# Kernel tuning notes

Measured on AMD Instinct MI355X. Metric: run time of the kernel, lower is better.

## Reference

```python
import jax, jax.numpy as jnp
import numpy as np

N_NODES = 100000
N_EDGES = 1600000
N_CONCEPTS = 500000
D = 128  # concept_dim = graph_hidden_dim = graph_output_dim


def setup_inputs() -> dict:
    key = jax.random.key(0)
    ks = jax.random.split(key, 10)
    cncpt_ids = jax.random.randint(ks[0], (N_NODES,), 0, N_CONCEPTS)
    src = jax.random.randint(ks[1], (N_EDGES,), 0, N_NODES)
    dst = jax.random.randint(ks[2], (N_EDGES,), 0, N_NODES)
    emb_table = jax.random.normal(ks[3], (N_CONCEPTS, D), dtype=jnp.float32)
    W1 = jax.random.normal(ks[4], (D, D), dtype=jnp.float32) * 0.05
    b1 = jax.random.normal(ks[5], (D,), dtype=jnp.float32) * 0.05
    W2 = jax.random.normal(ks[6], (D, D), dtype=jnp.float32) * 0.05
    b2 = jax.random.normal(ks[7], (D,), dtype=jnp.float32) * 0.05
    Wout = jax.random.normal(ks[8], (1, D), dtype=jnp.float32) * 0.05
    bout = jax.random.normal(ks[9], (1,), dtype=jnp.float32) * 0.05
    return {"cncpt_ids": cncpt_ids, "src": src, "dst": dst,
            "emb_table": emb_table, "W1": W1, "b1": b1,
            "W2": W2, "b2": b2, "Wout": Wout, "bout": bout}


def _gcn_layer(h, src, dst, W, b, n_nodes):
    # DGL update_all(copy_src, sum): gather messages from src, sum into dst
    agg = jax.ops.segment_sum(h[src], dst, num_segments=n_nodes)  # [N, d_in]
    return jax.nn.relu(agg @ W.T + b)  # NodeApplyModule: Linear + ReLU


def reference(cncpt_ids, src, dst, emb_table, W1, b1, W2, b2, Wout, bout):
    n_nodes = cncpt_ids.shape[0]
    h = emb_table[cncpt_ids]                       # [N, D] concept embeddings
    h = _gcn_layer(h, src, dst, W1, b1, n_nodes)   # gcn1
    h = _gcn_layer(h, src, dst, W2, b2, n_nodes)   # gcn2
    x = h[None]                                    # torch.stack([h]) -> [1, N, D]
    logits = jax.nn.sigmoid(x @ Wout.T + bout)     # hidden2output -> [1, N, 1]
    return logits
```

## Files before the change

### kernel.cpp

```cpp
#include <hip/hip_runtime.h>
#include <math.h>

#define D 128
#define SCAN_B 256

typedef __attribute__((ext_vector_type(8))) short bfrag;
typedef __attribute__((ext_vector_type(4))) float ffrag;

__device__ inline unsigned short f2bf(float f) {
    unsigned u = __float_as_uint(f);
    u += 0x7FFF + ((u >> 16) & 1);
    return (unsigned short)(u >> 16);
}
__device__ inline float bf2f(unsigned short h) {
    return __uint_as_float(((unsigned)h) << 16);
}
__device__ inline unsigned pack_bf2(float a, float b) {
    return ((unsigned)f2bf(a)) | (((unsigned)f2bf(b)) << 16);
}

__global__ void setup1_kernel(const float* __restrict__ W1,
                              const float* __restrict__ W2,
                              unsigned short* __restrict__ hi1,
                              unsigned short* __restrict__ lo1,
                              unsigned short* __restrict__ hi2,
                              unsigned short* __restrict__ lo2,
                              int* __restrict__ deg, int np1, int nblk_w) {
    if ((int)blockIdx.x < nblk_w) {
        int i = blockIdx.x * blockDim.x + threadIdx.x;
        if (i < D * D) {
            float f1 = W1[i];
            unsigned short h1 = f2bf(f1);
            hi1[i] = h1;
            lo1[i] = f2bf(f1 - bf2f(h1));
            float f2 = W2[i];
            unsigned short h2 = f2bf(f2);
            hi2[i] = h2;
            lo2[i] = f2bf(f2 - bf2f(h2));
        }
    } else {
        int i = ((int)blockIdx.x - nblk_w) * blockDim.x + threadIdx.x;
        if (i < np1) deg[i] = 0;
    }
}

__global__ void setup2_kernel(const float* __restrict__ emb,
                              const int* __restrict__ ids,
                              uint4* __restrict__ h4,
                              const int* __restrict__ dst,
                              int* __restrict__ deg,
                              int n_nodes, int n_edges, int nblk_g) {
    if ((int)blockIdx.x < nblk_g) {
        int idx = blockIdx.x * blockDim.x + threadIdx.x;
        int total = n_nodes * 16;
        if (idx >= total) return;
        int node = idx >> 4;
        int c = idx & 15;
        size_t cid = (size_t)ids[node];
        const float4* s = (const float4*)(emb + cid * D) + c * 2;
        float4 v0 = s[0];
        float4 v1 = s[1];
        uint4 p;
        p.x = pack_bf2(v0.x, v0.y);
        p.y = pack_bf2(v0.z, v0.w);
        p.z = pack_bf2(v1.x, v1.y);
        p.w = pack_bf2(v1.z, v1.w);
        h4[(size_t)node * 16 + c] = p;
    } else {
        int e = ((int)blockIdx.x - nblk_g) * blockDim.x + threadIdx.x;
        if (e < n_edges) atomicAdd(&deg[dst[e]], 1);
    }
}

__global__ __launch_bounds__(SCAN_B) void scan_block_kernel(
        const int* __restrict__ deg, int* __restrict__ row_ptr,
        int* __restrict__ blocksums, int n) {
    __shared__ int s[SCAN_B];
    int i = blockIdx.x * SCAN_B + threadIdx.x;
    int v = (i < n) ? deg[i] : 0;
    s[threadIdx.x] = v;
    __syncthreads();
    #pragma unroll
    for (int off = 1; off < SCAN_B; off <<= 1) {
        int t = (threadIdx.x >= off) ? s[threadIdx.x - off] : 0;
        __syncthreads();
        s[threadIdx.x] += t;
        __syncthreads();
    }
    if (i < n) row_ptr[i] = s[threadIdx.x] - v;
    if (threadIdx.x == SCAN_B - 1) blocksums[blockIdx.x] = s[SCAN_B - 1];
}

__global__ __launch_bounds__(512) void scan_sums_kernel(int* __restrict__ blocksums,
                                                        int nb) {
    __shared__ int s[512];
    int v = (threadIdx.x < nb) ? blocksums[threadIdx.x] : 0;
    s[threadIdx.x] = v;
    __syncthreads();
    #pragma unroll
    for (int off = 1; off < 512; off <<= 1) {
        int t = (threadIdx.x >= off) ? s[threadIdx.x - off] : 0;
        __syncthreads();
        s[threadIdx.x] += t;
        __syncthreads();
    }
    if (threadIdx.x < nb) blocksums[threadIdx.x] = s[threadIdx.x] - v;
}

__global__ void add_offsets_kernel(int* __restrict__ row_ptr,
                                   const int* __restrict__ blocksums,
                                   int* __restrict__ cursor, int n, int n_nodes) {
    int i = blockIdx.x * blockDim.x + threadIdx.x;
    if (i >= n) return;
    int rp = row_ptr[i] + blocksums[i / SCAN_B];
    row_ptr[i] = rp;
    if (i < n_nodes) cursor[i] = rp;
}

__global__ void csr_fill_kernel(const int* __restrict__ src,
                                const int* __restrict__ dst,
                                int* __restrict__ cursor,
                                int* __restrict__ esrc, int n_edges) {
    int e = blockIdx.x * blockDim.x + threadIdx.x;
    if (e >= n_edges) return;
    int pos = atomicAdd(&cursor[dst[e]], 1);
    esrc[pos] = src[e];
}

#define ACC8(u) do { \
    a0 += __uint_as_float((u).x << 16); a1 += __uint_as_float((u).x & 0xffff0000u); \
    a2 += __uint_as_float((u).y << 16); a3 += __uint_as_float((u).y & 0xffff0000u); \
    a4 += __uint_as_float((u).z << 16); a5 += __uint_as_float((u).z & 0xffff0000u); \
    a6 += __uint_as_float((u).w << 16); a7 += __uint_as_float((u).w & 0xffff0000u); \
} while (0)

__global__ __launch_bounds__(256) void agg_kernel(
        const uint4* __restrict__ h4, const int* __restrict__ row_ptr,
        const int* __restrict__ esrc, uint4* __restrict__ agg4, int n_nodes) {
    int node = blockIdx.x * 4 + (threadIdx.x >> 6);
    int lane = threadIdx.x & 63;
    if (node >= n_nodes) return;
    const int c = lane & 15;
    const int g = lane >> 4;
    int beg = row_ptr[node], end = row_ptr[node + 1];
    int deg = end - beg;

    int myidx = 0;
    if (lane < deg) myidx = esrc[beg + lane];

    float a0 = 0.f, a1 = 0.f, a2 = 0.f, a3 = 0.f;
    float a4 = 0.f, a5 = 0.f, a6 = 0.f, a7 = 0.f;

    int nfast = deg < 64 ? deg : 64;
    for (int base = 0; base < nfast; base += 16) {
        int p0 = base + g;
        int s0 = __shfl(myidx, p0, 64);
        int s1 = __shfl(myidx, p0 + 4, 64);
        int s2 = __shfl(myidx, p0 + 8, 64);
        int s3 = __shfl(myidx, p0 + 12, 64);
        bool v0 = p0 < nfast;
        bool v1 = (p0 + 4) < nfast;
        bool v2 = (p0 + 8) < nfast;
        bool v3 = (p0 + 12) < nfast;
        uint4 u0, u1, u2, u3;
        if (v0) u0 = h4[(size_t)s0 * 16 + c];
        if (v1) u1 = h4[(size_t)s1 * 16 + c];
        if (v2) u2 = h4[(size_t)s2 * 16 + c];
        if (v3) u3 = h4[(size_t)s3 * 16 + c];
        if (v0) ACC8(u0);
        if (v1) ACC8(u1);
        if (v2) ACC8(u2);
        if (v3) ACC8(u3);
    }
    for (int i = beg + 64 + g; i < end; i += 4) {
        uint4 u = h4[(size_t)esrc[i] * 16 + c];
        ACC8(u);
    }

    a0 += __shfl_xor(a0, 16, 64); a0 += __shfl_xor(a0, 32, 64);
    a1 += __shfl_xor(a1, 16, 64); a1 += __shfl_xor(a1, 32, 64);
    a2 += __shfl_xor(a2, 16, 64); a2 += __shfl_xor(a2, 32, 64);
    a3 += __shfl_xor(a3, 16, 64); a3 += __shfl_xor(a3, 32, 64);
    a4 += __shfl_xor(a4, 16, 64); a4 += __shfl_xor(a4, 32, 64);
    a5 += __shfl_xor(a5, 16, 64); a5 += __shfl_xor(a5, 32, 64);
    a6 += __shfl_xor(a6, 16, 64); a6 += __shfl_xor(a6, 32, 64);
    a7 += __shfl_xor(a7, 16, 64); a7 += __shfl_xor(a7, 32, 64);

    if (g == 0) {
        uint4 r;
        r.x = pack_bf2(a0, a1);
        r.y = pack_bf2(a2, a3);
        r.z = pack_bf2(a4, a5);
        r.w = pack_bf2(a6, a7);
        agg4[(size_t)node * 16 + c] = r;
    }
}

__global__ __launch_bounds__(256) void linear_mfma_kernel(
        const unsigned short* __restrict__ x,
        const unsigned short* __restrict__ Whi,
        const unsigned short* __restrict__ Wlo,
        const float* __restrict__ b,
        unsigned short* __restrict__ y,
        const float* __restrict__ wout,
        const float* __restrict__ bout,
        float* __restrict__ outp,
        int n_nodes, int fuse_out) {
    __shared__ __align__(16) unsigned short sW[2][D][136];

    {
        const uint4* Wh4 = (const uint4*)Whi;
        const uint4* Wl4 = (const uint4*)Wlo;
        #pragma unroll
        for (int j = 0; j < 8; ++j) {
            int ch = (int)threadIdx.x + j * 256;
            int row = ch >> 4, k8 = ch & 15;
            *(uint4*)&sW[0][row][k8 * 8] = Wh4[ch];
            *(uint4*)&sW[1][row][k8 * 8] = Wl4[ch];
        }
    }
    __syncthreads();

    const int lane = threadIdx.x & 63;
    const int col  = lane & 15;
    const int quad = lane >> 4;
    const int wave = blockIdx.x * 4 + (threadIdx.x >> 6);
    const int nwaves = gridDim.x * 4;
    const int ngroups = (n_nodes + 15) >> 4;

    float bvals[8], wvals[8];
    #pragma unroll
    for (int nt = 0; nt < 8; ++nt) {
        bvals[nt] = b[nt * 16 + col];
        wvals[nt] = fuse_out ? wout[nt * 16 + col] : 0.f;
    }
    const float bout0 = fuse_out ? bout[0] : 0.f;

    for (int g = wave; g < ngroups; g += nwaves) {
        int node = g * 16 + col;
        int nload = node < n_nodes ? node : (n_nodes - 1);

        bfrag a[4];
        #pragma unroll
        for (int kt = 0; kt < 4; ++kt)
            a[kt] = *(const bfrag*)(x + (size_t)nload * D + kt * 32 + quad * 8);

        float part0 = 0.f, part1 = 0.f, part2 = 0.f, part3 = 0.f;

        #pragma unroll
        for (int nt = 0; nt < 8; ++nt) {
            ffrag c = {0.f, 0.f, 0.f, 0.f};
            #pragma unroll
            for (int kt = 0; kt < 4; ++kt) {
                bfrag bh = *(const bfrag*)&sW[0][nt * 16 + col][kt * 32 + quad * 8];
                bfrag bl = *(const bfrag*)&sW[1][nt * 16 + col][kt * 32 + quad * 8];
                c = __builtin_amdgcn_mfma_f32_16x16x32_bf16(a[kt], bh, c, 0, 0, 0);
                c = __builtin_amdgcn_mfma_f32_16x16x32_bf16(a[kt], bl, c, 0, 0, 0);
            }
            if (fuse_out) {
                part0 += fmaxf(c[0] + bvals[nt], 0.f) * wvals[nt];
                part1 += fmaxf(c[1] + bvals[nt], 0.f) * wvals[nt];
                part2 += fmaxf(c[2] + bvals[nt], 0.f) * wvals[nt];
                part3 += fmaxf(c[3] + bvals[nt], 0.f) * wvals[nt];
            } else {
                #pragma unroll
                for (int r = 0; r < 4; ++r) {
                    int onode = g * 16 + quad * 4 + r;
                    if (onode < n_nodes)
                        y[(size_t)onode * D + nt * 16 + col] =
                            f2bf(fmaxf(c[r] + bvals[nt], 0.f));
                }
            }
        }

        if (fuse_out) {
            float part[4] = {part0, part1, part2, part3};
            #pragma unroll
            for (int r = 0; r < 4; ++r) {
                float s = part[r];
                s += __shfl_xor(s, 1, 64);
                s += __shfl_xor(s, 2, 64);
                s += __shfl_xor(s, 4, 64);
                s += __shfl_xor(s, 8, 64);
                int onode = g * 16 + quad * 4 + r;
                if (col == 0 && onode < n_nodes)
                    outp[onode] = 1.0f / (1.0f + expf(-(s + bout0)));
            }
        }
    }
}

extern "C" void kernel_launch(void* const* d_in, const int* in_sizes, int n_in,
                              void* d_out, int out_size, void* d_ws, size_t ws_size,
                              hipStream_t stream) {
    const int*   cncpt_ids = (const int*)d_in[0];
    const int*   src       = (const int*)d_in[1];
    const int*   dst       = (const int*)d_in[2];
    const float* emb       = (const float*)d_in[3];
    const float* W1        = (const float*)d_in[4];
    const float* b1        = (const float*)d_in[5];
    const float* W2        = (const float*)d_in[6];
    const float* b2        = (const float*)d_in[7];
    const float* Wout      = (const float*)d_in[8];
    const float* bout      = (const float*)d_in[9];
    float* out = (float*)d_out;

    const int n_nodes = in_sizes[0];
    const int n_edges = in_sizes[1];

    unsigned short* bufA = (unsigned short*)d_ws;
    unsigned short* bufB = bufA + (size_t)n_nodes * D;
    int*   deg      = (int*)(bufB + (size_t)n_nodes * D);
    int*   row_ptr  = deg + (n_nodes + 1);
    int*   cursor   = row_ptr + (n_nodes + 1);
    int*   blocksums= cursor + n_nodes;
    int*   esrc     = blocksums + 512;
    size_t walign   = ((size_t)(esrc + n_edges) + 15) & ~(size_t)15;
    unsigned short* W1hi = (unsigned short*)walign;
    unsigned short* W1lo = W1hi + D * D;
    unsigned short* W2hi = W1lo + D * D;
    unsigned short* W2lo = W2hi + D * D;

    const int np1 = n_nodes + 1;
    const int nb_scan = (np1 + SCAN_B - 1) / SCAN_B;

    const int nblk_w = (D * D + 255) / 256;
    const int nblk_z = (np1 + 255) / 256;
    setup1_kernel<<<nblk_w + nblk_z, 256, 0, stream>>>(
        W1, W2, W1hi, W1lo, W2hi, W2lo, deg, np1, nblk_w);

    const int nblk_g = (n_nodes * 16 + 255) / 256;
    const int nblk_d = (n_edges + 255) / 256;
    setup2_kernel<<<nblk_g + nblk_d, 256, 0, stream>>>(
        emb, cncpt_ids, (uint4*)bufA, dst, deg, n_nodes, n_edges, nblk_g);

    scan_block_kernel<<<nb_scan, SCAN_B, 0, stream>>>(deg, row_ptr, blocksums, np1);
    scan_sums_kernel<<<1, 512, 0, stream>>>(blocksums, nb_scan);
    add_offsets_kernel<<<(np1 + 255) / 256, 256, 0, stream>>>(
        row_ptr, blocksums, cursor, np1, n_nodes);
    csr_fill_kernel<<<nblk_d, 256, 0, stream>>>(src, dst, cursor, esrc, n_edges);

    const int agg_grid = (n_nodes + 3) / 4;
    const int ngroups = (n_nodes + 15) / 16;
    const int lin_grid = (ngroups + 7) / 8;

    agg_kernel<<<agg_grid, 256, 0, stream>>>(
        (const uint4*)bufA, row_ptr, esrc, (uint4*)bufB, n_nodes);
    linear_mfma_kernel<<<lin_grid, 256, 0, stream>>>(
        bufB, W1hi, W1lo, b1, bufA, nullptr, nullptr, nullptr, n_nodes, 0);

    agg_kernel<<<agg_grid, 256, 0, stream>>>(
        (const uint4*)bufA, row_ptr, esrc, (uint4*)bufB, n_nodes);
    linear_mfma_kernel<<<lin_grid, 256, 0, stream>>>(
        bufB, W2hi, W2lo, b2, nullptr, Wout, bout, out, n_nodes, 1);
}
```

Before: 674.3 us.

## Fuse all GCN stages into one cooperative persistent kernel with grid syncs

Replaces the chain of roughly ten kernel launches (setup, degree count, scan, CSR fill, two aggregation and two linear passes) with a single cooperative persistent kernel that separates the phases with grid-wide barriers, falling back to the old multi-launch path if the cooperative launch fails. The aim is to remove per-launch overhead and the idle gaps between dependent small kernels. The linear phase now stages only the high half of W in shared memory and reads the low half from global memory, which lowers shared-memory use and so allows more resident blocks. The costs are grid-sync latency, the serial single-block scan of block sums, grid-stride loops in every phase, and extra global reads of the low weights.

```diff
diff --git a/kernel.cpp b/kernel.cpp
--- a/kernel.cpp
+++ b/kernel.cpp
@@ -1,5 +1,8 @@
 #include <hip/hip_runtime.h>
+#include <hip/hip_cooperative_groups.h>
 #include <math.h>
+
+namespace cg = cooperative_groups;
 
 #define D 128
 #define SCAN_B 256
@@ -18,6 +21,309 @@
 __device__ inline unsigned pack_bf2(float a, float b) {
     return ((unsigned)f2bf(a)) | (((unsigned)f2bf(b)) << 16);
 }
+
+#define ACC8(u) do { \
+    a0 += __uint_as_float((u).x << 16); a1 += __uint_as_float((u).x & 0xffff0000u); \
+    a2 += __uint_as_float((u).y << 16); a3 += __uint_as_float((u).y & 0xffff0000u); \
+    a4 += __uint_as_float((u).z << 16); a5 += __uint_as_float((u).z & 0xffff0000u); \
+    a6 += __uint_as_float((u).w << 16); a7 += __uint_as_float((u).w & 0xffff0000u); \
+} while (0)
+
+
+__device__ __forceinline__ void agg_phase(
+        const uint4* __restrict__ h4, const int* __restrict__ row_ptr,
+        const int* __restrict__ esrc, uint4* __restrict__ agg4,
+        int n_nodes, int wave_gid, int nwaves) {
+    const int lane = threadIdx.x & 63;
+    const int c = lane & 15;
+    const int g = lane >> 4;
+
+    for (int node = wave_gid; node < n_nodes; node += nwaves) {
+        int beg = row_ptr[node], end = row_ptr[node + 1];
+        int deg = end - beg;
+
+        int myidx = 0;
+        if (lane < deg) myidx = esrc[beg + lane];
+
+        float a0 = 0.f, a1 = 0.f, a2 = 0.f, a3 = 0.f;
+        float a4 = 0.f, a5 = 0.f, a6 = 0.f, a7 = 0.f;
+
+        int nfast = deg < 64 ? deg : 64;
+        for (int base = 0; base < nfast; base += 16) {
+            int p0 = base + g;
+            int s0 = __shfl(myidx, p0, 64);
+            int s1 = __shfl(myidx, p0 + 4, 64);
+            int s2 = __shfl(myidx, p0 + 8, 64);
+            int s3 = __shfl(myidx, p0 + 12, 64);
+            bool v0 = p0 < nfast;
+            bool v1 = (p0 + 4) < nfast;
+            bool v2 = (p0 + 8) < nfast;
+            bool v3 = (p0 + 12) < nfast;
+            uint4 u0, u1, u2, u3;
+            if (v0) u0 = h4[(size_t)s0 * 16 + c];
+            if (v1) u1 = h4[(size_t)s1 * 16 + c];
+            if (v2) u2 = h4[(size_t)s2 * 16 + c];
+            if (v3) u3 = h4[(size_t)s3 * 16 + c];
+            if (v0) ACC8(u0);
+            if (v1) ACC8(u1);
+            if (v2) ACC8(u2);
+            if (v3) ACC8(u3);
+        }
+        for (int i = beg + 64 + g; i < end; i += 4) {
+            uint4 u = h4[(size_t)esrc[i] * 16 + c];
+            ACC8(u);
+        }
+
+        a0 += __shfl_xor(a0, 16, 64); a0 += __shfl_xor(a0, 32, 64);
+        a1 += __shfl_xor(a1, 16, 64); a1 += __shfl_xor(a1, 32, 64);
+        a2 += __shfl_xor(a2, 16, 64); a2 += __shfl_xor(a2, 32, 64);
+        a3 += __shfl_xor(a3, 16, 64); a3 += __shfl_xor(a3, 32, 64);
+        a4 += __shfl_xor(a4, 16, 64); a4 += __shfl_xor(a4, 32, 64);
+        a5 += __shfl_xor(a5, 16, 64); a5 += __shfl_xor(a5, 32, 64);
+        a6 += __shfl_xor(a6, 16, 64); a6 += __shfl_xor(a6, 32, 64);
+        a7 += __shfl_xor(a7, 16, 64); a7 += __shfl_xor(a7, 32, 64);
+
+        if (g == 0) {
+            uint4 r;
+            r.x = pack_bf2(a0, a1);
+            r.y = pack_bf2(a2, a3);
+            r.z = pack_bf2(a4, a5);
+            r.w = pack_bf2(a6, a7);
+            agg4[(size_t)node * 16 + c] = r;
+        }
+    }
+}
+
+__device__ __forceinline__ void linear_phase(
+        const unsigned short* __restrict__ x,
+        const unsigned short* __restrict__ swhi,
+        const unsigned short* __restrict__ Wlo,
+        const float* __restrict__ b,
+        unsigned short* __restrict__ y,
+        const float* __restrict__ wout,
+        const float* __restrict__ bout,
+        float* __restrict__ outp,
+        int n_nodes, int fuse_out, int wave_gid, int nwaves) {
+    const int lane = threadIdx.x & 63;
+    const int col  = lane & 15;
+    const int quad = lane >> 4;
+    const int ngroups = (n_nodes + 15) >> 4;
+
+    float bvals[8], wvals[8];
+    #pragma unroll
+    for (int nt = 0; nt < 8; ++nt) {
+        bvals[nt] = b[nt * 16 + col];
+        wvals[nt] = fuse_out ? wout[nt * 16 + col] : 0.f;
+    }
+    const float bout0 = fuse_out ? bout[0] : 0.f;
+
+    for (int g = wave_gid; g < ngroups; g += nwaves) {
+        int node = g * 16 + col;
+        int nload = node < n_nodes ? node : (n_nodes - 1);
+
+        bfrag a[4];
+        #pragma unroll
+        for (int kt = 0; kt < 4; ++kt)
+            a[kt] = *(const bfrag*)(x + (size_t)nload * D + kt * 32 + quad * 8);
+
+        float part0 = 0.f, part1 = 0.f, part2 = 0.f, part3 = 0.f;
+
+        #pragma unroll
+        for (int nt = 0; nt < 8; ++nt) {
+            ffrag c = {0.f, 0.f, 0.f, 0.f};
+            #pragma unroll
+            for (int kt = 0; kt < 4; ++kt) {
+                bfrag bh = *(const bfrag*)&swhi[(nt * 16 + col) * 136 + kt * 32 + quad * 8];
+                bfrag bl = *(const bfrag*)(Wlo + (size_t)(nt * 16 + col) * D + kt * 32 + quad * 8);
+                c = __builtin_amdgcn_mfma_f32_16x16x32_bf16(a[kt], bh, c, 0, 0, 0);
+                c = __builtin_amdgcn_mfma_f32_16x16x32_bf16(a[kt], bl, c, 0, 0, 0);
+            }
+            if (fuse_out) {
+                part0 += fmaxf(c[0] + bvals[nt], 0.f) * wvals[nt];
+                part1 += fmaxf(c[1] + bvals[nt], 0.f) * wvals[nt];
+                part2 += fmaxf(c[2] + bvals[nt], 0.f) * wvals[nt];
+                part3 += fmaxf(c[3] + bvals[nt], 0.f) * wvals[nt];
+            } else {
+                #pragma unroll
+                for (int r = 0; r < 4; ++r) {
+                    int onode = g * 16 + quad * 4 + r;
+                    if (onode < n_nodes)
+                        y[(size_t)onode * D + nt * 16 + col] =
+                            f2bf(fmaxf(c[r] + bvals[nt], 0.f));
+                }
+            }
+        }
+
+        if (fuse_out) {
+            float part[4] = {part0, part1, part2, part3};
+            #pragma unroll
+            for (int r = 0; r < 4; ++r) {
+                float s = part[r];
+                s += __shfl_xor(s, 1, 64);
+                s += __shfl_xor(s, 2, 64);
+                s += __shfl_xor(s, 4, 64);
+                s += __shfl_xor(s, 8, 64);
+                int onode = g * 16 + quad * 4 + r;
+                if (col == 0 && onode < n_nodes)
+                    outp[onode] = 1.0f / (1.0f + expf(-(s + bout0)));
+            }
+        }
+    }
+}
+
+
+struct MegaParams {
+    const int* cncpt_ids; const int* src; const int* dst;
+    const float* emb;
+    const float* W1; const float* b1;
+    const float* W2; const float* b2;
+    const float* Wout; const float* bout;
+    float* out;
+    unsigned short* bufA; unsigned short* bufB;
+    unsigned short* W1hi; unsigned short* W1lo;
+    unsigned short* W2hi; unsigned short* W2lo;
+    int* deg; int* row_ptr; int* cursor; int* blocksums; int* esrc;
+    int n_nodes; int n_edges;
+};
+
+union __align__(16) SMem {
+    int scan[512];
+    unsigned short w[128 * 136];
+};
+
+__device__ __forceinline__ void stage_whi(unsigned short* w,
+                                          const unsigned short* __restrict__ Whi) {
+    const uint4* s4 = (const uint4*)Whi;
+    #pragma unroll
+    for (int j = 0; j < 8; ++j) {
+        int ch = (int)threadIdx.x + j * 256;
+        int row = ch >> 4, k8 = ch & 15;
+        *(uint4*)&w[row * 136 + k8 * 8] = s4[ch];
+    }
+}
+
+__global__ __launch_bounds__(256, 4) void mega_kernel(MegaParams p) {
+    __shared__ SMem sm;
+    cg::grid_group grd = cg::this_grid();
+    const int tid  = threadIdx.x;
+    const int gtid = (int)blockIdx.x * 256 + tid;
+    const int gsz  = (int)gridDim.x * 256;
+    const int wave_gid = gtid >> 6;
+    const int nwaves   = gsz >> 6;
+    const int np1 = p.n_nodes + 1;
+    const int nb  = (np1 + SCAN_B - 1) / SCAN_B;
+
+    for (int i = gtid; i < D * D; i += gsz) {
+        float f1 = p.W1[i];
+        unsigned short h1 = f2bf(f1);
+        p.W1hi[i] = h1;
+        p.W1lo[i] = f2bf(f1 - bf2f(h1));
+        float f2 = p.W2[i];
+        unsigned short h2 = f2bf(f2);
+        p.W2hi[i] = h2;
+        p.W2lo[i] = f2bf(f2 - bf2f(h2));
+    }
+    for (int i = gtid; i < np1; i += gsz) p.deg[i] = 0;
+    for (int idx = gtid; idx < p.n_nodes * 16; idx += gsz) {
+        int node = idx >> 4;
+        int c = idx & 15;
+        size_t cid = (size_t)p.cncpt_ids[node];
+        const float4* s = (const float4*)(p.emb + cid * D) + c * 2;
+        float4 v0 = s[0];
+        float4 v1 = s[1];
+        uint4 pk;
+        pk.x = pack_bf2(v0.x, v0.y);
+        pk.y = pack_bf2(v0.z, v0.w);
+        pk.z = pack_bf2(v1.x, v1.y);
+        pk.w = pack_bf2(v1.z, v1.w);
+        ((uint4*)p.bufA)[(size_t)node * 16 + c] = pk;
+    }
+    __threadfence();
+    grd.sync();
+
+    for (int e = gtid; e < p.n_edges; e += gsz) atomicAdd(&p.deg[p.dst[e]], 1);
+    __threadfence();
+    grd.sync();
+
+    for (int vb = (int)blockIdx.x; vb < nb; vb += (int)gridDim.x) {
+        int i = vb * SCAN_B + tid;
+        int v = (i < np1) ? p.deg[i] : 0;
+        sm.scan[tid] = v;
+        __syncthreads();
+        #pragma unroll
+        for (int off = 1; off < SCAN_B; off <<= 1) {
+            int t = (tid >= off) ? sm.scan[tid - off] : 0;
+            __syncthreads();
+            sm.scan[tid] += t;
+            __syncthreads();
+        }
+        if (i < np1) p.row_ptr[i] = sm.scan[tid] - v;
+        if (tid == SCAN_B - 1) p.blocksums[vb] = sm.scan[SCAN_B - 1];
+        __syncthreads();
+    }
+    __threadfence();
+    grd.sync();
+
+    if (blockIdx.x == 0) {
+        int carry = 0;
+        for (int c0 = 0; c0 < nb; c0 += 256) {
+            int i = c0 + tid;
+            int v = (i < nb) ? p.blocksums[i] : 0;
+            sm.scan[tid] = v;
+            __syncthreads();
+            #pragma unroll
+            for (int off = 1; off < 256; off <<= 1) {
+                int t = (tid >= off) ? sm.scan[tid - off] : 0;
+                __syncthreads();
+                sm.scan[tid] += t;
+                __syncthreads();
+            }
+            if (i < nb) p.blocksums[i] = sm.scan[tid] - v + carry;
+            carry += sm.scan[255];
+            __syncthreads();
+        }
+    }
+    __threadfence();
+    grd.sync();
+
+    for (int i = gtid; i < np1; i += gsz) {
+        int rp = p.row_ptr[i] + p.blocksums[i / SCAN_B];
+        p.row_ptr[i] = rp;
+        if (i < p.n_nodes) p.cursor[i] = rp;
+    }
+    __threadfence();
+    grd.sync();
+
+    for (int e = gtid; e < p.n_edges; e += gsz) {
+        int pos = atomicAdd(&p.cursor[p.dst[e]], 1);
+        p.esrc[pos] = p.src[e];
+    }
+    __threadfence();
+    grd.sync();
+
+    agg_phase((const uint4*)p.bufA, p.row_ptr, p.esrc, (uint4*)p.bufB,
+              p.n_nodes, wave_gid, nwaves);
+    __threadfence();
+    grd.sync();
+
+    stage_whi(sm.w, p.W1hi);
+    __syncthreads();
+    linear_phase(p.bufB, sm.w, p.W1lo, p.b1, p.bufA,
+                 nullptr, nullptr, nullptr, p.n_nodes, 0, wave_gid, nwaves);
+    __threadfence();
+    grd.sync();
+
+    agg_phase((const uint4*)p.bufA, p.row_ptr, p.esrc, (uint4*)p.bufB,
+              p.n_nodes, wave_gid, nwaves);
+    __threadfence();
+    grd.sync();
+
+    stage_whi(sm.w, p.W2hi);
+    __syncthreads();
+    linear_phase(p.bufB, sm.w, p.W2lo, p.b2, nullptr,
+                 p.Wout, p.bout, p.out, p.n_nodes, 1, wave_gid, nwaves);
+}
+
 
 __global__ void setup1_kernel(const float* __restrict__ W1,
                               const float* __restrict__ W2,
@@ -60,12 +366,12 @@
         const float4* s = (const float4*)(emb + cid * D) + c * 2;
         float4 v0 = s[0];
         float4 v1 = s[1];
-        uint4 p;
-        p.x = pack_bf2(v0.x, v0.y);
-        p.y = pack_bf2(v0.z, v0.w);
-        p.z = pack_bf2(v1.x, v1.y);
-        p.w = pack_bf2(v1.z, v1.w);
-        h4[(size_t)node * 16 + c] = p;
+        uint4 pk;
+        pk.x = pack_bf2(v0.x, v0.y);
+        pk.y = pack_bf2(v0.z, v0.w);
+        pk.z = pack_bf2(v1.x, v1.y);
+        pk.w = pack_bf2(v1.z, v1.w);
+        h4[(size_t)node * 16 + c] = pk;
     } else {
         int e = ((int)blockIdx.x - nblk_g) * blockDim.x + threadIdx.x;
         if (e < n_edges) atomicAdd(&deg[dst[e]], 1);
@@ -127,73 +433,12 @@
     esrc[pos] = src[e];
 }
 
-#define ACC8(u) do { \
-    a0 += __uint_as_float((u).x << 16); a1 += __uint_as_float((u).x & 0xffff0000u); \
-    a2 += __uint_as_float((u).y << 16); a3 += __uint_as_float((u).y & 0xffff0000u); \
-    a4 += __uint_as_float((u).z << 16); a5 += __uint_as_float((u).z & 0xffff0000u); \
-    a6 += __uint_as_float((u).w << 16); a7 += __uint_as_float((u).w & 0xffff0000u); \
-} while (0)
-
 __global__ __launch_bounds__(256) void agg_kernel(
         const uint4* __restrict__ h4, const int* __restrict__ row_ptr,
         const int* __restrict__ esrc, uint4* __restrict__ agg4, int n_nodes) {
-    int node = blockIdx.x * 4 + (threadIdx.x >> 6);
-    int lane = threadIdx.x & 63;
-    if (node >= n_nodes) return;
-    const int c = lane & 15;
-    const int g = lane >> 4;
-    int beg = row_ptr[node], end = row_ptr[node + 1];
-    int deg = end - beg;
-
-    int myidx = 0;
-    if (lane < deg) myidx = esrc[beg + lane];
-
-    float a0 = 0.f, a1 = 0.f, a2 = 0.f, a3 = 0.f;
-    float a4 = 0.f, a5 = 0.f, a6 = 0.f, a7 = 0.f;
-
-    int nfast = deg < 64 ? deg : 64;
-    for (int base = 0; base < nfast; base += 16) {
-        int p0 = base + g;
-        int s0 = __shfl(myidx, p0, 64);
-        int s1 = __shfl(myidx, p0 + 4, 64);
-        int s2 = __shfl(myidx, p0 + 8, 64);
-        int s3 = __shfl(myidx, p0 + 12, 64);
-        bool v0 = p0 < nfast;
-        bool v1 = (p0 + 4) < nfast;
-        bool v2 = (p0 + 8) < nfast;
-        bool v3 = (p0 + 12) < nfast;
-        uint4 u0, u1, u2, u3;
-        if (v0) u0 = h4[(size_t)s0 * 16 + c];
-        if (v1) u1 = h4[(size_t)s1 * 16 + c];
-        if (v2) u2 = h4[(size_t)s2 * 16 + c];
-        if (v3) u3 = h4[(size_t)s3 * 16 + c];
-        if (v0) ACC8(u0);
-        if (v1) ACC8(u1);
-        if (v2) ACC8(u2);
-        if (v3) ACC8(u3);
-    }
-    for (int i = beg + 64 + g; i < end; i += 4) {
-        uint4 u = h4[(size_t)esrc[i] * 16 + c];
-        ACC8(u);
-    }
-
-    a0 += __shfl_xor(a0, 16, 64); a0 += __shfl_xor(a0, 32, 64);
-    a1 += __shfl_xor(a1, 16, 64); a1 += __shfl_xor(a1, 32, 64);
-    a2 += __shfl_xor(a2, 16, 64); a2 += __shfl_xor(a2, 32, 64);
-    a3 += __shfl_xor(a3, 16, 64); a3 += __shfl_xor(a3, 32, 64);
-    a4 += __shfl_xor(a4, 16, 64); a4 += __shfl_xor(a4, 32, 64);
-    a5 += __shfl_xor(a5, 16, 64); a5 += __shfl_xor(a5, 32, 64);
-    a6 += __shfl_xor(a6, 16, 64); a6 += __shfl_xor(a6, 32, 64);
-    a7 += __shfl_xor(a7, 16, 64); a7 += __shfl_xor(a7, 32, 64);
-
-    if (g == 0) {
-        uint4 r;
-        r.x = pack_bf2(a0, a1);
-        r.y = pack_bf2(a2, a3);
-        r.z = pack_bf2(a4, a5);
-        r.w = pack_bf2(a6, a7);
-        agg4[(size_t)node * 16 + c] = r;
-    }
+    int wave_gid = (int)(blockIdx.x * 4 + (threadIdx.x >> 6));
+    if (wave_gid >= n_nodes) return;
+    agg_phase(h4, row_ptr, esrc, agg4, n_nodes, wave_gid, (int)gridDim.x * 4);
 }
 
 __global__ __launch_bounds__(256) void linear_mfma_kernel(
@@ -206,89 +451,14 @@
         const float* __restrict__ bout,
         float* __restrict__ outp,
         int n_nodes, int fuse_out) {
-    __shared__ __align__(16) unsigned short sW[2][D][136];
-
-    {
-        const uint4* Wh4 = (const uint4*)Whi;
-        const uint4* Wl4 = (const uint4*)Wlo;
-        #pragma unroll
-        for (int j = 0; j < 8; ++j) {
-            int ch = (int)threadIdx.x + j * 256;
-            int row = ch >> 4, k8 = ch & 15;
-            *(uint4*)&sW[0][row][k8 * 8] = Wh4[ch];
-            *(uint4*)&sW[1][row][k8 * 8] = Wl4[ch];
-        }
-    }
+    __shared__ __align__(16) unsigned short sW[128 * 136];
+    stage_whi(sW, Whi);
     __syncthreads();
-
-    const int lane = threadIdx.x & 63;
-    const int col  = lane & 15;
-    const int quad = lane >> 4;
-    const int wave = blockIdx.x * 4 + (threadIdx.x >> 6);
-    const int nwaves = gridDim.x * 4;
-    const int ngroups = (n_nodes + 15) >> 4;
-
-    float bvals[8], wvals[8];
-    #pragma unroll
-    for (int nt = 0; nt < 8; ++nt) {
-        bvals[nt] = b[nt * 16 + col];
-        wvals[nt] = fuse_out ? wout[nt * 16 + col] : 0.f;
-    }
-    const float bout0 = fuse_out ? bout[0] : 0.f;
-
-    for (int g = wave; g < ngroups; g += nwaves) {
-        int node = g * 16 + col;
-        int nload = node < n_nodes ? node : (n_nodes - 1);
-
-        bfrag a[4];
-        #pragma unroll
-        for (int kt = 0; kt < 4; ++kt)
-            a[kt] = *(const bfrag*)(x + (size_t)nload * D + kt * 32 + quad * 8);
-
-        float part0 = 0.f, part1 = 0.f, part2 = 0.f, part3 = 0.f;
-
-        #pragma unroll
-        for (int nt = 0; nt < 8; ++nt) {
-            ffrag c = {0.f, 0.f, 0.f, 0.f};
-            #pragma unroll
-            for (int kt = 0; kt < 4; ++kt) {
-                bfrag bh = *(const bfrag*)&sW[0][nt * 16 + col][kt * 32 + quad * 8];
-                bfrag bl = *(const bfrag*)&sW[1][nt * 16 + col][kt * 32 + quad * 8];
-                c = __builtin_amdgcn_mfma_f32_16x16x32_bf16(a[kt], bh, c, 0, 0, 0);
-                c = __builtin_amdgcn_mfma_f32_16x16x32_bf16(a[kt], bl, c, 0, 0, 0);
-            }
-            if (fuse_out) {
-                part0 += fmaxf(c[0] + bvals[nt], 0.f) * wvals[nt];
-                part1 += fmaxf(c[1] + bvals[nt], 0.f) * wvals[nt];
-                part2 += fmaxf(c[2] + bvals[nt], 0.f) * wvals[nt];
-                part3 += fmaxf(c[3] + bvals[nt], 0.f) * wvals[nt];
-            } else {
-                #pragma unroll
-                for (int r = 0; r < 4; ++r) {
-                    int onode = g * 16 + quad * 4 + r;
-                    if (onode < n_nodes)
-                        y[(size_t)onode * D + nt * 16 + col] =
-                            f2bf(fmaxf(c[r] + bvals[nt], 0.f));
-                }
-            }
-        }
-
-        if (fuse_out) {
-            float part[4] = {part0, part1, part2, part3};
-            #pragma unroll
-            for (int r = 0; r < 4; ++r) {
-                float s = part[r];
-                s += __shfl_xor(s, 1, 64);
-                s += __shfl_xor(s, 2, 64);
-                s += __shfl_xor(s, 4, 64);
-                s += __shfl_xor(s, 8, 64);
-                int onode = g * 16 + quad * 4 + r;
-                if (col == 0 && onode < n_nodes)
-                    outp[onode] = 1.0f / (1.0f + expf(-(s + bout0)));
-            }
-        }
-    }
-}
+    int wave_gid = (int)(blockIdx.x * 4 + (threadIdx.x >> 6));
+    linear_phase(x, sW, Wlo, b, y, wout, bout, outp, n_nodes, fuse_out,
+                 wave_gid, (int)gridDim.x * 4);
+}
+
 
 extern "C" void kernel_launch(void* const* d_in, const int* in_sizes, int n_in,
                               void* d_out, int out_size, void* d_ws, size_t ws_size,
@@ -324,6 +494,27 @@
     const int np1 = n_nodes + 1;
     const int nb_scan = (np1 + SCAN_B - 1) / SCAN_B;
 
+    MegaParams p;
+    p.cncpt_ids = cncpt_ids; p.src = src; p.dst = dst; p.emb = emb;
+    p.W1 = W1; p.b1 = b1; p.W2 = W2; p.b2 = b2; p.Wout = Wout; p.bout = bout;
+    p.out = out;
+    p.bufA = bufA; p.bufB = bufB;
+    p.W1hi = W1hi; p.W1lo = W1lo; p.W2hi = W2hi; p.W2lo = W2lo;
+    p.deg = deg; p.row_ptr = row_ptr; p.cursor = cursor;
+    p.blocksums = blocksums; p.esrc = esrc;
+    p.n_nodes = n_nodes; p.n_edges = n_edges;
+
+    int maxb = 0;
+    hipError_t oerr = hipOccupancyMaxActiveBlocksPerMultiprocessor(
+        &maxb, mega_kernel, 256, 0);
+    int grid = (oerr == hipSuccess && maxb > 0) ? maxb * 256 : 512;
+    if (grid > 2048) grid = 2048;
+
+    void* args[] = {(void*)&p};
+    hipError_t lerr = hipLaunchCooperativeKernel(
+        mega_kernel, dim3(grid), dim3(256), args, 0, stream);
+    if (lerr == hipSuccess) return;
+
     const int nblk_w = (D * D + 255) / 256;
     const int nblk_z = (np1 + 255) / 256;
     setup1_kernel<<<nblk_w + nblk_z, 256, 0, stream>>>(
```

Result: slower. 1.800 ms (+166.9%).

## Fuse neighbor aggregation with MFMA linear layer using persistent atomic work queue

Applied to the files above, without the earlier changes.

Merges the aggregation kernel and the linear MFMA kernel into one persistent kernel per layer. Each wave takes 16-node groups from an atomic counter, gathers and sums neighbor rows into a swizzled LDS tile, then runs the bf16 hi/lo MFMA directly on that tile. This removes the write and re-read of the aggregate buffer through global memory and two launches. It also unrolls the gather to 8 loads in flight, stores only W_hi in LDS with an XOR swizzle, and reads W_lo from global/L2. The trade-offs are fewer resident waves for latency hiding, serialized gather and MFMA phases within a wave, and extra global traffic for W_lo.

```diff
diff --git a/kernel.cpp b/kernel.cpp
--- a/kernel.cpp
+++ b/kernel.cpp
@@ -18,6 +18,15 @@
 __device__ inline unsigned pack_bf2(float a, float b) {
     return ((unsigned)f2bf(a)) | (((unsigned)f2bf(b)) << 16);
 }
+
+#define XSWZ(row, off) ((off) ^ (((row) & 7) << 3))
+
+#define ACC8(u) do { \
+    a0 += __uint_as_float((u).x << 16); a1 += __uint_as_float((u).x & 0xffff0000u); \
+    a2 += __uint_as_float((u).y << 16); a3 += __uint_as_float((u).y & 0xffff0000u); \
+    a4 += __uint_as_float((u).z << 16); a5 += __uint_as_float((u).z & 0xffff0000u); \
+    a6 += __uint_as_float((u).w << 16); a7 += __uint_as_float((u).w & 0xffff0000u); \
+} while (0)
 
 __global__ void setup1_kernel(const float* __restrict__ W1,
                               const float* __restrict__ W2,
@@ -25,7 +34,8 @@
                               unsigned short* __restrict__ lo1,
                               unsigned short* __restrict__ hi2,
                               unsigned short* __restrict__ lo2,
-                              int* __restrict__ deg, int np1, int nblk_w) {
+                              int* __restrict__ deg, int* __restrict__ wcnt,
+                              int np1, int nblk_w) {
     if ((int)blockIdx.x < nblk_w) {
         int i = blockIdx.x * blockDim.x + threadIdx.x;
         if (i < D * D) {
@@ -41,6 +51,7 @@
     } else {
         int i = ((int)blockIdx.x - nblk_w) * blockDim.x + threadIdx.x;
         if (i < np1) deg[i] = 0;
+        if (i < 2) wcnt[i] = 0;
     }
 }
 
@@ -127,77 +138,10 @@
     esrc[pos] = src[e];
 }
 
-#define ACC8(u) do { \
-    a0 += __uint_as_float((u).x << 16); a1 += __uint_as_float((u).x & 0xffff0000u); \
-    a2 += __uint_as_float((u).y << 16); a3 += __uint_as_float((u).y & 0xffff0000u); \
-    a4 += __uint_as_float((u).z << 16); a5 += __uint_as_float((u).z & 0xffff0000u); \
-    a6 += __uint_as_float((u).w << 16); a7 += __uint_as_float((u).w & 0xffff0000u); \
-} while (0)
-
-__global__ __launch_bounds__(256) void agg_kernel(
-        const uint4* __restrict__ h4, const int* __restrict__ row_ptr,
-        const int* __restrict__ esrc, uint4* __restrict__ agg4, int n_nodes) {
-    int node = blockIdx.x * 4 + (threadIdx.x >> 6);
-    int lane = threadIdx.x & 63;
-    if (node >= n_nodes) return;
-    const int c = lane & 15;
-    const int g = lane >> 4;
-    int beg = row_ptr[node], end = row_ptr[node + 1];
-    int deg = end - beg;
-
-    int myidx = 0;
-    if (lane < deg) myidx = esrc[beg + lane];
-
-    float a0 = 0.f, a1 = 0.f, a2 = 0.f, a3 = 0.f;
-    float a4 = 0.f, a5 = 0.f, a6 = 0.f, a7 = 0.f;
-
-    int nfast = deg < 64 ? deg : 64;
-    for (int base = 0; base < nfast; base += 16) {
-        int p0 = base + g;
-        int s0 = __shfl(myidx, p0, 64);
-        int s1 = __shfl(myidx, p0 + 4, 64);
-        int s2 = __shfl(myidx, p0 + 8, 64);
-        int s3 = __shfl(myidx, p0 + 12, 64);
-        bool v0 = p0 < nfast;
-        bool v1 = (p0 + 4) < nfast;
-        bool v2 = (p0 + 8) < nfast;
-        bool v3 = (p0 + 12) < nfast;
-        uint4 u0, u1, u2, u3;
-        if (v0) u0 = h4[(size_t)s0 * 16 + c];
-        if (v1) u1 = h4[(size_t)s1 * 16 + c];
-        if (v2) u2 = h4[(size_t)s2 * 16 + c];
-        if (v3) u3 = h4[(size_t)s3 * 16 + c];
-        if (v0) ACC8(u0);
-        if (v1) ACC8(u1);
-        if (v2) ACC8(u2);
-        if (v3) ACC8(u3);
-    }
-    for (int i = beg + 64 + g; i < end; i += 4) {
-        uint4 u = h4[(size_t)esrc[i] * 16 + c];
-        ACC8(u);
-    }
-
-    a0 += __shfl_xor(a0, 16, 64); a0 += __shfl_xor(a0, 32, 64);
-    a1 += __shfl_xor(a1, 16, 64); a1 += __shfl_xor(a1, 32, 64);
-    a2 += __shfl_xor(a2, 16, 64); a2 += __shfl_xor(a2, 32, 64);
-    a3 += __shfl_xor(a3, 16, 64); a3 += __shfl_xor(a3, 32, 64);
-    a4 += __shfl_xor(a4, 16, 64); a4 += __shfl_xor(a4, 32, 64);
-    a5 += __shfl_xor(a5, 16, 64); a5 += __shfl_xor(a5, 32, 64);
-    a6 += __shfl_xor(a6, 16, 64); a6 += __shfl_xor(a6, 32, 64);
-    a7 += __shfl_xor(a7, 16, 64); a7 += __shfl_xor(a7, 32, 64);
-
-    if (g == 0) {
-        uint4 r;
-        r.x = pack_bf2(a0, a1);
-        r.y = pack_bf2(a2, a3);
-        r.z = pack_bf2(a4, a5);
-        r.w = pack_bf2(a6, a7);
-        agg4[(size_t)node * 16 + c] = r;
-    }
-}
-
-__global__ __launch_bounds__(256) void linear_mfma_kernel(
-        const unsigned short* __restrict__ x,
+__global__ __launch_bounds__(512, 4) void fused_layer_kernel(
+        const uint4* __restrict__ h4,
+        const int* __restrict__ row_ptr,
+        const int* __restrict__ esrc,
         const unsigned short* __restrict__ Whi,
         const unsigned short* __restrict__ Wlo,
         const float* __restrict__ b,
@@ -205,70 +149,148 @@
         const float* __restrict__ wout,
         const float* __restrict__ bout,
         float* __restrict__ outp,
+        int* __restrict__ wcnt,
         int n_nodes, int fuse_out) {
-    __shared__ __align__(16) unsigned short sW[2][D][136];
-
+    __shared__ __align__(16) unsigned short sW[128 * 128];
+    __shared__ __align__(16) unsigned short sX[8][16 * 128];
+
+    const int tid = threadIdx.x;
     {
-        const uint4* Wh4 = (const uint4*)Whi;
-        const uint4* Wl4 = (const uint4*)Wlo;
+        const uint4* s4 = (const uint4*)Whi;
         #pragma unroll
-        for (int j = 0; j < 8; ++j) {
-            int ch = (int)threadIdx.x + j * 256;
+        for (int j = 0; j < 4; ++j) {
+            int ch = tid + j * 512;
             int row = ch >> 4, k8 = ch & 15;
-            *(uint4*)&sW[0][row][k8 * 8] = Wh4[ch];
-            *(uint4*)&sW[1][row][k8 * 8] = Wl4[ch];
+            *(uint4*)&sW[row * 128 + XSWZ(row, k8 * 8)] = s4[ch];
         }
     }
     __syncthreads();
 
-    const int lane = threadIdx.x & 63;
-    const int col  = lane & 15;
-    const int quad = lane >> 4;
-    const int wave = blockIdx.x * 4 + (threadIdx.x >> 6);
-    const int nwaves = gridDim.x * 4;
+    const int wid  = tid >> 6;
+    const int lane = tid & 63;
+    const int c    = lane & 15;
+    const int g    = lane >> 4;
+    unsigned short* xt = &sX[wid][0];
     const int ngroups = (n_nodes + 15) >> 4;
 
     float bvals[8], wvals[8];
     #pragma unroll
     for (int nt = 0; nt < 8; ++nt) {
-        bvals[nt] = b[nt * 16 + col];
-        wvals[nt] = fuse_out ? wout[nt * 16 + col] : 0.f;
+        bvals[nt] = b[nt * 16 + c];
+        wvals[nt] = fuse_out ? wout[nt * 16 + c] : 0.f;
     }
     const float bout0 = fuse_out ? bout[0] : 0.f;
 
-    for (int g = wave; g < ngroups; g += nwaves) {
-        int node = g * 16 + col;
-        int nload = node < n_nodes ? node : (n_nodes - 1);
+    for (;;) {
+        int grp;
+        if (lane == 0) grp = atomicAdd(wcnt, 1);
+        grp = __shfl(grp, 0, 64);
+        if (grp >= ngroups) break;
+
+        for (int j = 0; j < 16; ++j) {
+            int node = grp * 16 + j;
+            int beg = 0, end = 0;
+            if (node < n_nodes) { beg = row_ptr[node]; end = row_ptr[node + 1]; }
+            int deg = end - beg;
+            int myidx = 0;
+            if (lane < deg) myidx = esrc[beg + lane];
+
+            float a0 = 0.f, a1 = 0.f, a2 = 0.f, a3 = 0.f;
+            float a4 = 0.f, a5 = 0.f, a6 = 0.f, a7 = 0.f;
+
+            int nfast = deg < 64 ? deg : 64;
+            for (int base = 0; base < nfast; base += 32) {
+                int p0 = base + g;
+                int p4 = p0 + 16;
+                int s0 = __shfl(myidx, p0, 64);
+                int s1 = __shfl(myidx, p0 + 4, 64);
+                int s2 = __shfl(myidx, p0 + 8, 64);
+                int s3 = __shfl(myidx, p0 + 12, 64);
+                int s4i = __shfl(myidx, p4, 64);
+                int s5 = __shfl(myidx, p4 + 4, 64);
+                int s6 = __shfl(myidx, p4 + 8, 64);
+                int s7 = __shfl(myidx, p4 + 12, 64);
+                bool v0 = p0 < nfast;
+                bool v1 = (p0 + 4) < nfast;
+                bool v2 = (p0 + 8) < nfast;
+                bool v3 = (p0 + 12) < nfast;
+                bool v4 = p4 < nfast;
+                bool v5 = (p4 + 4) < nfast;
+                bool v6 = (p4 + 8) < nfast;
+                bool v7 = (p4 + 12) < nfast;
+                uint4 u0, u1, u2, u3, u4, u5, u6, u7;
+                if (v0) u0 = h4[(size_t)s0 * 16 + c];
+                if (v1) u1 = h4[(size_t)s1 * 16 + c];
+                if (v2) u2 = h4[(size_t)s2 * 16 + c];
+                if (v3) u3 = h4[(size_t)s3 * 16 + c];
+                if (v4) u4 = h4[(size_t)s4i * 16 + c];
+                if (v5) u5 = h4[(size_t)s5 * 16 + c];
+                if (v6) u6 = h4[(size_t)s6 * 16 + c];
+                if (v7) u7 = h4[(size_t)s7 * 16 + c];
+                if (v0) ACC8(u0);
+                if (v1) ACC8(u1);
+                if (v2) ACC8(u2);
+                if (v3) ACC8(u3);
+                if (v4) ACC8(u4);
+                if (v5) ACC8(u5);
+                if (v6) ACC8(u6);
+                if (v7) ACC8(u7);
+            }
+            for (int i = beg + 64 + g; i < end; i += 4) {
+                uint4 u = h4[(size_t)esrc[i] * 16 + c];
+                ACC8(u);
+            }
+
+            a0 += __shfl_xor(a0, 16, 64); a0 += __shfl_xor(a0, 32, 64);
+            a1 += __shfl_xor(a1, 16, 64); a1 += __shfl_xor(a1, 32, 64);
+            a2 += __shfl_xor(a2, 16, 64); a2 += __shfl_xor(a2, 32, 64);
+            a3 += __shfl_xor(a3, 16, 64); a3 += __shfl_xor(a3, 32, 64);
+            a4 += __shfl_xor(a4, 16, 64); a4 += __shfl_xor(a4, 32, 64);
+            a5 += __shfl_xor(a5, 16, 64); a5 += __shfl_xor(a5, 32, 64);
+            a6 += __shfl_xor(a6, 16, 64); a6 += __shfl_xor(a6, 32, 64);
+            a7 += __shfl_xor(a7, 16, 64); a7 += __shfl_xor(a7, 32, 64);
+
+            if (g == 0) {
+                uint4 r;
+                r.x = pack_bf2(a0, a1);
+                r.y = pack_bf2(a2, a3);
+                r.z = pack_bf2(a4, a5);
+                r.w = pack_bf2(a6, a7);
+                *(uint4*)&xt[j * 128 + XSWZ(j, c * 8)] = r;
+            }
+        }
+        __asm__ volatile("s_waitcnt lgkmcnt(0)" ::: "memory");
 
         bfrag a[4];
         #pragma unroll
         for (int kt = 0; kt < 4; ++kt)
-            a[kt] = *(const bfrag*)(x + (size_t)nload * D + kt * 32 + quad * 8);
+            a[kt] = *(const bfrag*)&xt[c * 128 + XSWZ(c, kt * 32 + g * 8)];
 
         float part0 = 0.f, part1 = 0.f, part2 = 0.f, part3 = 0.f;
 
         #pragma unroll
         for (int nt = 0; nt < 8; ++nt) {
-            ffrag c = {0.f, 0.f, 0.f, 0.f};
+            ffrag cc = {0.f, 0.f, 0.f, 0.f};
             #pragma unroll
             for (int kt = 0; kt < 4; ++kt) {
-                bfrag bh = *(const bfrag*)&sW[0][nt * 16 + col][kt * 32 + quad * 8];
-                bfrag bl = *(const bfrag*)&sW[1][nt * 16 + col][kt * 32 + quad * 8];
-                c = __builtin_amdgcn_mfma_f32_16x16x32_bf16(a[kt], bh, c, 0, 0, 0);
-                c = __builtin_amdgcn_mfma_f32_16x16x32_bf16(a[kt], bl, c, 0, 0, 0);
+                int o = nt * 16 + c;
+                bfrag bh = *(const bfrag*)&sW[o * 128 + XSWZ(o, kt * 32 + g * 8)];
+                bfrag bl = *(const bfrag*)(Wlo + (size_t)o * D + kt * 32 + g * 8);
+                cc = __builtin_amdgcn_mfma_f32_16x16x32_bf16(a[kt], bh, cc, 0, 0, 0);
+                cc = __builtin_amdgcn_mfma_f32_16x16x32_bf16(a[kt], bl, cc, 0, 0, 0);
             }
             if (fuse_out) {
-                part0 += fmaxf(c[0] + bvals[nt], 0.f) * wvals[nt];
-                part1 += fmaxf(c[1] + bvals[nt], 0.f) * wvals[nt];
-                part2 += fmaxf(c[2] + bvals[nt], 0.f) * wvals[nt];
-                part3 += fmaxf(c[3] + bvals[nt], 0.f) * wvals[nt];
+                part0 += fmaxf(cc[0] + bvals[nt], 0.f) * wvals[nt];
+                part1 += fmaxf(cc[1] + bvals[nt], 0.f) * wvals[nt];
+                part2 += fmaxf(cc[2] + bvals[nt], 0.f) * wvals[nt];
+                part3 += fmaxf(cc[3] + bvals[nt], 0.f) * wvals[nt];
             } else {
                 #pragma unroll
                 for (int r = 0; r < 4; ++r) {
-                    int onode = g * 16 + quad * 4 + r;
+                    int onode = grp * 16 + g * 4 + r;
                     if (onode < n_nodes)
-                        y[(size_t)onode * D + nt * 16 + col] =
-                            f2bf(fmaxf(c[r] + bvals[nt], 0.f));
+                        y[(size_t)onode * D + nt * 16 + c] =
+                            f2bf(fmaxf(cc[r] + bvals[nt], 0.f));
                 }
             }
         }
@@ -282,13 +304,14 @@
                 s += __shfl_xor(s, 2, 64);
                 s += __shfl_xor(s, 4, 64);
                 s += __shfl_xor(s, 8, 64);
-                int onode = g * 16 + quad * 4 + r;
-                if (col == 0 && onode < n_nodes)
+                int onode = grp * 16 + g * 4 + r;
+                if (c == 0 && onode < n_nodes)
                     outp[onode] = 1.0f / (1.0f + expf(-(s + bout0)));
             }
         }
     }
 }
+
 
 extern "C" void kernel_launch(void* const* d_in, const int* in_sizes, int n_in,
                               void* d_out, int out_size, void* d_ws, size_t ws_size,
@@ -314,6 +337,7 @@
     int*   row_ptr  = deg + (n_nodes + 1);
     int*   cursor   = row_ptr + (n_nodes + 1);
     int*   blocksums= cursor + n_nodes;
+    int*   wcnt     = blocksums + 504;
     int*   esrc     = blocksums + 512;
     size_t walign   = ((size_t)(esrc + n_edges) + 15) & ~(size_t)15;
     unsigned short* W1hi = (unsigned short*)walign;
@@ -327,7 +351,7 @@
     const int nblk_w = (D * D + 255) / 256;
     const int nblk_z = (np1 + 255) / 256;
     setup1_kernel<<<nblk_w + nblk_z, 256, 0, stream>>>(
-        W1, W2, W1hi, W1lo, W2hi, W2lo, deg, np1, nblk_w);
+        W1, W2, W1hi, W1lo, W2hi, W2lo, deg, wcnt, np1, nblk_w);
 
     const int nblk_g = (n_nodes * 16 + 255) / 256;
     const int nblk_d = (n_edges + 255) / 256;
@@ -340,17 +364,15 @@
         row_ptr, blocksums, cursor, np1, n_nodes);
     csr_fill_kernel<<<nblk_d, 256, 0, stream>>>(src, dst, cursor, esrc, n_edges);
 
-    const int agg_grid = (n_nodes + 3) / 4;
     const int ngroups = (n_nodes + 15) / 16;
-    const int lin_grid = (ngroups + 7) / 8;
-
-    agg_kernel<<<agg_grid, 256, 0, stream>>>(
-        (const uint4*)bufA, row_ptr, esrc, (uint4*)bufB, n_nodes);
-    linear_mfma_kernel<<<lin_grid, 256, 0, stream>>>(
-        bufB, W1hi, W1lo, b1, bufA, nullptr, nullptr, nullptr, n_nodes, 0);
-
-    agg_kernel<<<agg_grid, 256, 0, stream>>>(
-        (const uint4*)bufA, row_ptr, esrc, (uint4*)bufB, n_nodes);
-    linear_mfma_kernel<<<lin_grid, 256, 0, stream>>>(
-        bufB, W2hi, W2lo, b2, nullptr, Wout, bout, out, n_nodes, 1);
-}
+    int fgrid = 512;
+    if (fgrid > ngroups) fgrid = ngroups;
+
+    fused_layer_kernel<<<fgrid, 512, 0, stream>>>(
+        (const uint4*)bufA, row_ptr, esrc, W1hi, W1lo, b1,
+        bufB, nullptr, nullptr, nullptr, wcnt + 0, n_nodes, 0);
+
+    fused_layer_kernel<<<fgrid, 512, 0, stream>>>(
+        (const uint4*)bufB, row_ptr, esrc, W2hi, W2lo, b2,
+        nullptr, Wout, bout, out, wcnt + 1, n_nodes, 1);
+}
```

Result: slower. 866.3 us (+28.5%).
